# Kernel optimization log

Hardware: AMD Instinct MI355X
Metric: run time of the kernel (lower is better)

Reference implementation:

```python
import jax, jax.numpy as jnp
import numpy as np

B, S, D, H = 2, 2048, 4096, 32
HD = D // H  # 128

def _rope(t, cos, sin):
    # t: [B,S,H,HD]; cos,sin: [S,HD//2]; interleaved complex pairs on last dim
    b, s, h, d = t.shape
    tr = t.reshape(b, s, h, d // 2, 2)
    x0, x1 = tr[..., 0], tr[..., 1]
    c = cos[None, :, None, :]
    sn = sin[None, :, None, :]
    o0 = x0 * c - x1 * sn
    o1 = x0 * sn + x1 * c
    return jnp.stack([o0, o1], axis=-1).reshape(b, s, h, d)

def setup_inputs() -> dict:
    key = jax.random.key(0)
    ks = jax.random.split(key, 6)
    x = jax.random.normal(ks[0], (B, S, D), dtype=jnp.float32)
    theta = 10000.0 ** (-jnp.arange(0, HD, 2, dtype=jnp.float32) / HD)  # [HD//2]
    ang = jnp.arange(S, dtype=jnp.float32)[:, None] * theta[None, :]    # [S, HD//2]
    freqs_cos, freqs_sin = jnp.cos(ang), jnp.sin(ang)
    # additive causal mask [S,S]
    mask = jnp.where(jnp.triu(jnp.ones((S, S), dtype=bool), k=1), -1e9, 0.0).astype(jnp.float32)
    std = 1.0 / np.sqrt(D)
    wq = jax.random.normal(ks[1], (D, D), dtype=jnp.float32) * std
    wk = jax.random.normal(ks[2], (D, D), dtype=jnp.float32) * std
    wv = jax.random.normal(ks[3], (D, D), dtype=jnp.float32) * std
    wo = jax.random.normal(ks[4], (D, D), dtype=jnp.float32) * std
    return {"x": x, "freqs_cos": freqs_cos, "freqs_sin": freqs_sin, "mask": mask,
            "wq": wq, "wk": wk, "wv": wv, "wo": wo, "start_pos": 0}

def reference(x, freqs_cos, freqs_sin, mask, wq, wk, wv, wo, start_pos):
    b, s, d = x.shape
    # Linear layers: torch nn.Linear stores weight [out,in] -> x @ W.T
    xq = (x @ wq.T).reshape(b, s, H, HD)
    xk = (x @ wk.T).reshape(b, s, H, HD)
    xv = (x @ wv.T).reshape(b, s, H, HD)
    xq = _rope(xq, freqs_cos, freqs_sin)
    xk = _rope(xk, freqs_cos, freqs_sin)
    # prefill (start_pos=0): cache slice [:, :s] == xk, xv
    scale = 1.0 / jnp.sqrt(jnp.float32(HD))
    scores = jnp.einsum("bqhd,bkhd->bhqk", xq, xk) * scale + mask[None, None, :, :]
    probs = jax.nn.softmax(scores, axis=-1)
    out = jnp.einsum("bhqk,bkhd->bqhd", probs, xv).reshape(b, s, d)
    return out @ wo.T
```

## Files before the change

### kernel.cpp

```cpp
#include <hip/hip_runtime.h>
#include <hip/hip_bf16.h>
#include <math.h>

typedef unsigned short u16;
typedef __bf16 bf16x8 __attribute__((ext_vector_type(8)));
typedef float f32x4 __attribute__((ext_vector_type(4)));

#define B_  2
#define S_  2048
#define D_  4096
#define H_  32
#define HD_ 128

__device__ __forceinline__ unsigned rne_bf16(float x) {
  unsigned u = __float_as_uint(x);
  return (u + 0x7fffu + ((u >> 16) & 1u)) >> 16;
}

__device__ __forceinline__ void async16(void* lds_p, const void* g) {
  __builtin_amdgcn_global_load_lds(
      (__attribute__((address_space(1))) void*)(g),
      (__attribute__((address_space(3))) void*)(lds_p), 16, 0, 0);
}

__global__ __launch_bounds__(256) void convert_bf16(
    const float* __restrict__ src, u16* __restrict__ dst, int n8) {
  int i = blockIdx.x * 256 + threadIdx.x;
  if (i >= n8) return;
  const float4* s = (const float4*)src + (size_t)i * 2;
  float4 a = s[0], b = s[1];
  uint4 o;
  o.x = rne_bf16(a.x) | (rne_bf16(a.y) << 16);
  o.y = rne_bf16(a.z) | (rne_bf16(a.w) << 16);
  o.z = rne_bf16(b.x) | (rne_bf16(b.y) << 16);
  o.w = rne_bf16(b.z) | (rne_bf16(b.w) << 16);
  ((uint4*)dst)[i] = o;
}

__global__ __launch_bounds__(256) void convert_bf16_x4(
    const float* __restrict__ s0, const float* __restrict__ s1,
    const float* __restrict__ s2, const float* __restrict__ s3,
    u16* __restrict__ d0, u16* __restrict__ d1,
    u16* __restrict__ d2, u16* __restrict__ d3) {
  const int per = (B_ * S_ * D_) / 8 / 256;
  const int which = blockIdx.x / per;
  const int i = (blockIdx.x % per) * 256 + threadIdx.x;
  const float* src = which == 0 ? s0 : which == 1 ? s1 : which == 2 ? s2 : s3;
  u16* dst = which == 0 ? d0 : which == 1 ? d1 : which == 2 ? d2 : d3;
  const float4* s = (const float4*)src + (size_t)i * 2;
  float4 a = s[0], b = s[1];
  uint4 o;
  o.x = rne_bf16(a.x) | (rne_bf16(a.y) << 16);
  o.y = rne_bf16(a.z) | (rne_bf16(a.w) << 16);
  o.z = rne_bf16(b.x) | (rne_bf16(b.y) << 16);
  o.w = rne_bf16(b.z) | (rne_bf16(b.w) << 16);
  ((uint4*)dst)[i] = o;
}

template <int MODE>
__global__ __launch_bounds__(256, 3) void gemm_bt(
    const u16* __restrict__ A, const u16* __restrict__ Bw,
    u16* __restrict__ outB, float* __restrict__ outF,
    const float* __restrict__ fc, const float* __restrict__ fs) {
  __shared__ __align__(16) u16 lds[24576];
  const int tid  = threadIdx.x;
  const int lane = tid & 63;
  const int wave = tid >> 6;
  const int lm   = lane & 15, quad = lane >> 4;
  const int mr = (wave >> 1) * 64, nc = (wave & 1) * 64;
  const int K = 4096;
  const int NT = K / 32;

  const int bid = blockIdx.y * 32 + blockIdx.x;
  const int xg = bid & 7, l = bid >> 3;
  const int m0 = (((xg & 3) * 8) + (l & 7)) * 128;
  const int n0 = (((xg >> 2) * 16) + (l >> 3)) * 128;

  const int ca = tid, cb = tid + 256;
  const int ra = ca >> 2, ga = ((ca & 3) ^ ((ca >> 3) & 3)) * 8;
  const int rb = cb >> 2, gb = ((cb & 3) ^ ((cb >> 3) & 3)) * 8;
  const u16* Ag0 = A + (size_t)(m0 + ra) * K + ga;
  const u16* Ag1 = A + (size_t)(m0 + rb) * K + gb;
  const u16* Bg0 = Bw + (size_t)(n0 + ra) * K + ga;
  const u16* Bg1 = Bw + (size_t)(n0 + rb) * K + gb;

  const int koff = (quad ^ ((lm >> 1) & 3)) * 8;

  f32x4 acc[4][4] = {};

#define GSTAGE(BUF, T) do {                                   \
    u16* Ld_ = lds + (BUF) * 8192;                            \
    const size_t ko_ = (size_t)(T) * 32;                      \
    async16(&Ld_[ca * 8], Ag0 + ko_);                         \
    async16(&Ld_[cb * 8], Ag1 + ko_);                         \
    async16(&Ld_[4096 + ca * 8], Bg0 + ko_);                  \
    async16(&Ld_[4096 + cb * 8], Bg1 + ko_);                  \
  } while (0)

  GSTAGE(0, 0);
  GSTAGE(1, 1);
  asm volatile("s_waitcnt vmcnt(4)" ::: "memory");
  asm volatile("s_barrier" ::: "memory");

  int rbuf = 0, sbuf = 2;
  for (int t = 0; t < NT; ++t) {
    const u16* As = lds + rbuf * 8192;
    const u16* Bs = As + 4096;
    if (t + 2 < NT) GSTAGE(sbuf, t + 2);
    bf16x8 af[4], bfr[4];
#pragma unroll
    for (int i = 0; i < 4; ++i) af[i] = *(const bf16x8*)&As[(mr + i * 16 + lm) * 32 + koff];
#pragma unroll
    for (int j = 0; j < 4; ++j) bfr[j] = *(const bf16x8*)&Bs[(nc + j * 16 + lm) * 32 + koff];
#pragma unroll
    for (int i = 0; i < 4; ++i)
#pragma unroll
      for (int j = 0; j < 4; ++j)
        acc[i][j] = __builtin_amdgcn_mfma_f32_16x16x32_bf16(af[i], bfr[j], acc[i][j], 0, 0, 0);
    if (t < NT - 1) {
      if (t + 2 < NT) {
        asm volatile("s_waitcnt vmcnt(4)" ::: "memory");
      } else {
        asm volatile("s_waitcnt vmcnt(0)" ::: "memory");
      }
      asm volatile("s_barrier" ::: "memory");
    }
    rbuf = rbuf == 2 ? 0 : rbuf + 1;
    sbuf = sbuf == 2 ? 0 : sbuf + 1;
  }
#undef GSTAGE

  if (MODE == 1) {
#pragma unroll
    for (int i = 0; i < 4; ++i) {
      const int mbase = m0 + mr + i * 16 + quad * 4;
#pragma unroll
      for (int j = 0; j < 4; ++j) {
        const int n = n0 + nc + j * 16 + lm;
        const int h = n >> 7, d = n & 127, ir = d >> 1;
#pragma unroll
        for (int r = 0; r < 4; ++r) {
          const int m = mbase + r;
          const int s = m & (S_ - 1);
          const int bb = m >> 11;
          float v = acc[i][j][r];
          float p = __shfl_xor(v, 1);
          float cv = fc[s * (HD_ / 2) + ir];
          float sv = fs[s * (HD_ / 2) + ir];
          float o = ((lane & 1) == 0) ? (v * cv - p * sv) : (p * sv + v * cv);
          float po = __shfl_xor(o, 1);
          if ((lane & 1) == 0) {
            unsigned pkt = rne_bf16(o) | (rne_bf16(po) << 16);
            size_t idx = (((size_t)(bb * H_ + h) * S_ + s) * HD_ + d) >> 1;
            ((unsigned*)outB)[idx] = pkt;
          }
        }
      }
    }
  } else if (MODE == 3) {
#pragma unroll
    for (int i = 0; i < 4; ++i) {
      const int mbase = m0 + mr + i * 16 + quad * 4;
      const int s0 = mbase & (S_ - 1);
      const int bb = mbase >> 11;
#pragma unroll
      for (int j = 0; j < 4; ++j) {
        const int n = n0 + nc + j * 16 + lm;
        const int h = n >> 7, d = n & 127;
        uint2 pkt;
        pkt.x = rne_bf16(acc[i][j][0]) | (rne_bf16(acc[i][j][1]) << 16);
        pkt.y = rne_bf16(acc[i][j][2]) | (rne_bf16(acc[i][j][3]) << 16);
        size_t idx = ((size_t)(bb * H_ + h) * HD_ + d) * S_ + s0;
        *(uint2*)&outB[idx] = pkt;
      }
    }
  } else {
#pragma unroll
    for (int i = 0; i < 4; ++i) {
      const int mbase = m0 + mr + i * 16 + quad * 4;
#pragma unroll
      for (int j = 0; j < 4; ++j) {
        const int n = n0 + nc + j * 16 + lm;
#pragma unroll
        for (int r = 0; r < 4; ++r) outF[(size_t)(mbase + r) * D_ + n] = acc[i][j][r];
      }
    }
  }
}

__global__ __launch_bounds__(256, 2) void flash_attn(
    const u16* __restrict__ Qb, const u16* __restrict__ Kb,
    const u16* __restrict__ Vtb, u16* __restrict__ attn) {
  __shared__ __align__(16) u16 lds[32768];

  const int tid = threadIdx.x;
  const int lane = tid & 63, w = tid >> 6;
  const int lm = lane & 15, quad = lane >> 4;
  const int qb = 15 - blockIdx.x;
  const int bh = blockIdx.y;
  const int bb = bh >> 5, h = bh & 31;

  const u16* Qg = Qb + ((size_t)bh * S_ + qb * 128 + w * 32) * HD_;
  const u16* Kg = Kb + (size_t)bh * S_ * HD_;
  const u16* Vg = Vtb + (size_t)bh * HD_ * S_;

  const u16* kp[4];
  const u16* vp[4];
#pragma unroll
  for (int it = 0; it < 4; ++it) {
    int c = tid + 256 * it;
    int kr = c >> 4, kc = (c & 15) ^ (kr & 15);
    kp[it] = Kg + (size_t)kr * HD_ + kc * 8;
    int vr = c >> 3, vc = (c & 7) ^ (vr & 7);
    vp[it] = Vg + (size_t)vr * S_ + vc * 8;
  }

  bf16x8 qf[2][4];
#pragma unroll
  for (int qt = 0; qt < 2; ++qt)
#pragma unroll
    for (int dk = 0; dk < 4; ++dk)
      qf[qt][dk] = *(const bf16x8*)(Qg + (size_t)(qt * 16 + lm) * HD_ + dk * 32 + quad * 8);

  f32x4 accO[8][2] = {};
  float m_run[2] = {-1e30f, -1e30f}, l_run[2] = {0.f, 0.f};
  const float scale = 0.08838834764831845f;
  const float THR = 90.50966799187809f;
  const int nkt = 2 * qb + 2;
  const int qg0 = qb * 128 + w * 32;
  const int wq_max = qg0 + 31;

#pragma unroll
  for (int it = 0; it < 4; ++it) {
    async16(&lds[(tid + 256 * it) * 8], kp[it]);
    async16(&lds[8192 + (tid + 256 * it) * 8], vp[it]);
  }

  for (int kt = 0; kt < nkt; ++kt) {
    const int k0 = kt * 64;
    const int cur = (kt & 1) * 16384;
    __syncthreads();
    if (kt + 1 < nkt) {
      const int nxt = cur ^ 16384;
      const size_t koK = (size_t)(kt + 1) * 64 * HD_;
      const size_t koV = (size_t)(kt + 1) * 64;
#pragma unroll
      for (int it = 0; it < 4; ++it) {
        async16(&lds[nxt + (tid + 256 * it) * 8], kp[it] + koK);
        async16(&lds[nxt + 8192 + (tid + 256 * it) * 8], vp[it] + koV);
      }
    }
    if (k0 <= wq_max) {
      const u16* Ks = lds + cur;
      const u16* Vts = lds + cur + 8192;
      f32x4 sacc[2][4] = {};
#pragma unroll
      for (int dk = 0; dk < 4; ++dk) {
        bf16x8 kf[4];
#pragma unroll
        for (int t = 0; t < 4; ++t) {
          int row = (t >> 1) * 32 + ((lm >> 2) * 8) + ((t & 1) * 4) + (lm & 3);
          int ch = (dk * 4 + quad) ^ (row & 15);
          kf[t] = *(const bf16x8*)&Ks[(row * 16 + ch) * 8];
        }
        __builtin_amdgcn_s_setprio(1);
#pragma unroll
        for (int t = 0; t < 4; ++t)
#pragma unroll
          for (int qt = 0; qt < 2; ++qt)
            sacc[qt][t] = __builtin_amdgcn_mfma_f32_16x16x32_bf16(kf[t], qf[qt][dk], sacc[qt][t], 0, 0, 0);
        __builtin_amdgcn_s_setprio(0);
      }
      if (k0 + 63 > qg0) {
#pragma unroll
        for (int qt = 0; qt < 2; ++qt) {
          int q = qg0 + qt * 16 + lm;
#pragma unroll
          for (int t = 0; t < 4; ++t) {
            int kb = k0 + (t >> 1) * 32 + quad * 8 + (t & 1) * 4;
#pragma unroll
            for (int r = 0; r < 4; ++r)
              if (kb + r > q) sacc[qt][t][r] = -1e30f;
          }
        }
      }
      float tmaxv[2];
#pragma unroll
      for (int qt = 0; qt < 2; ++qt) {
        float tmax = sacc[qt][0][0];
#pragma unroll
        for (int t = 0; t < 4; ++t)
#pragma unroll
          for (int r = 0; r < 4; ++r) tmax = fmaxf(tmax, sacc[qt][t][r]);
        tmax = fmaxf(tmax, __shfl_xor(tmax, 16));
        tmax = fmaxf(tmax, __shfl_xor(tmax, 32));
        tmaxv[qt] = tmax;
      }
      bool needl = (tmaxv[0] - m_run[0] > THR) || (tmaxv[1] - m_run[1] > THR);
      if (__any(needl)) {
#pragma unroll
        for (int qt = 0; qt < 2; ++qt) {
          float mnew = fmaxf(m_run[qt], tmaxv[qt]);
          float alpha = __expf((m_run[qt] - mnew) * scale);
          m_run[qt] = mnew;
          l_run[qt] *= alpha;
#pragma unroll
          for (int dt = 0; dt < 8; ++dt)
#pragma unroll
            for (int r = 0; r < 4; ++r) accO[dt][qt][r] *= alpha;
        }
      }
      bf16x8 pf[2][2];
#pragma unroll
      for (int qt = 0; qt < 2; ++qt) {
        float ms = m_run[qt] * scale;
        float rs = 0.f;
#pragma unroll
        for (int t = 0; t < 4; ++t)
#pragma unroll
          for (int r = 0; r < 4; ++r) {
            float p = __expf(fmaf(sacc[qt][t][r], scale, -ms));
            sacc[qt][t][r] = p;
            rs += p;
          }
        rs += __shfl_xor(rs, 16);
        rs += __shfl_xor(rs, 32);
        l_run[qt] += rs;
#pragma unroll
        for (int kc = 0; kc < 2; ++kc)
#pragma unroll
          for (int j = 0; j < 4; ++j) {
            pf[kc][qt][j]     = (__bf16)sacc[qt][2 * kc][j];
            pf[kc][qt][j + 4] = (__bf16)sacc[qt][2 * kc + 1][j];
          }
      }
      __builtin_amdgcn_s_setprio(1);
#pragma unroll
      for (int kc = 0; kc < 2; ++kc)
#pragma unroll
        for (int dt = 0; dt < 8; ++dt) {
          int row = dt * 16 + lm;
          int ch = (kc * 4 + quad) ^ (row & 7);
          bf16x8 vf = *(const bf16x8*)&Vts[(row * 8 + ch) * 8];
#pragma unroll
          for (int qt = 0; qt < 2; ++qt)
            accO[dt][qt] = __builtin_amdgcn_mfma_f32_16x16x32_bf16(vf, pf[kc][qt], accO[dt][qt], 0, 0, 0);
        }
      __builtin_amdgcn_s_setprio(0);
    }
  }

  __syncthreads();
  u16* Et = lds;
  float inv[2] = {1.f / l_run[0], 1.f / l_run[1]};
#pragma unroll
  for (int dt = 0; dt < 8; ++dt)
#pragma unroll
    for (int qt = 0; qt < 2; ++qt) {
      const int rowq = w * 32 + qt * 16 + lm;
#pragma unroll
      for (int rp = 0; rp < 2; ++rp) {
        float a0 = accO[dt][qt][rp * 2] * inv[qt];
        float a1 = accO[dt][qt][rp * 2 + 1] * inv[qt];
        unsigned pkt = rne_bf16(a0) | (rne_bf16(a1) << 16);
        *(unsigned*)&Et[rowq * 136 + dt * 16 + quad * 4 + rp * 2] = pkt;
      }
    }
  const int rloc = w * 32 + (lane >> 1);
  const int half = lane & 1;
  const size_t gbase = (size_t)(bb * S_ + qb * 128 + rloc) * D_ + h * 128 + half * 64;
#pragma unroll
  for (int k = 0; k < 8; ++k) {
    uint4 vv = *(const uint4*)&Et[rloc * 136 + half * 64 + k * 8];
    *(uint4*)&attn[gbase + k * 8] = vv;
  }
}

extern "C" void kernel_launch(void* const* d_in, const int* in_sizes, int n_in,
                              void* d_out, int out_size, void* d_ws, size_t ws_size,
                              hipStream_t stream) {
  const float* x  = (const float*)d_in[0];
  const float* fc = (const float*)d_in[1];
  const float* fs = (const float*)d_in[2];
  const float* wq = (const float*)d_in[4];
  const float* wk = (const float*)d_in[5];
  const float* wv = (const float*)d_in[6];
  const float* wo = (const float*)d_in[7];
  float* out = (float*)d_out;

  char* ws = (char*)d_ws;
  const size_t SZ = (size_t)B_ * S_ * D_ * 2;
  u16* xb  = (u16*)(ws);
  u16* wqb = (u16*)(ws + SZ);
  u16* wkb = (u16*)(ws + 2 * SZ);
  u16* wvb = (u16*)(ws + 3 * SZ);
  u16* Qb  = (u16*)(ws + 4 * SZ);
  u16* Kb  = (u16*)(ws + 5 * SZ);
  u16* Vtb = (u16*)(ws + 6 * SZ);
  u16* attn = xb;
  u16* wob  = wqb;

  dim3 blk(256);
  const int n8 = (B_ * S_ * D_) / 8;
  convert_bf16_x4<<<4 * (n8 / 256), blk, 0, stream>>>(x, wq, wk, wv, xb, wqb, wkb, wvb);

  dim3 g1(32, 32);
  gemm_bt<1><<<g1, blk, 0, stream>>>(xb, wqb, Qb, nullptr, fc, fs);
  gemm_bt<1><<<g1, blk, 0, stream>>>(xb, wkb, Kb, nullptr, fc, fs);
  gemm_bt<3><<<g1, blk, 0, stream>>>(xb, wvb, Vtb, nullptr, nullptr, nullptr);

  dim3 g2(16, 64);
  flash_attn<<<g2, blk, 0, stream>>>(Qb, Kb, Vtb, attn);

  convert_bf16<<<n8 / 256, blk, 0, stream>>>(wo, wob, n8);
  gemm_bt<4><<<g1, blk, 0, stream>>>(attn, wob, nullptr, out, nullptr, nullptr);
}
```

Baseline: 1.135 ms.

## Shrink LDS in GEMM and attention to raise occupancy

The GEMM drops from a three-stage to a two-stage LDS pipeline with a full barrier each k-step, cutting shared memory from 48KB to 32KB. The attention kernel double-buffers only K and single-buffers V, loading V for the current tile during QK^T and softmax, with an extra wait and barrier before PV. LDS drops to 48KB and launch bounds go to 3 blocks per CU. This trades prefetch depth and extra synchronisation for higher occupancy, and risks exposing load latency.

```diff
diff --git a/kernel.cpp b/kernel.cpp
--- a/kernel.cpp
+++ b/kernel.cpp
@@ -62,7 +62,7 @@
     const u16* __restrict__ A, const u16* __restrict__ Bw,
     u16* __restrict__ outB, float* __restrict__ outF,
     const float* __restrict__ fc, const float* __restrict__ fs) {
-  __shared__ __align__(16) u16 lds[24576];
+  __shared__ __align__(16) u16 lds[16384];
   const int tid  = threadIdx.x;
   const int lane = tid & 63;
   const int wave = tid >> 6;
@@ -88,25 +88,23 @@
 
   f32x4 acc[4][4] = {};
 
-#define GSTAGE(BUF, T) do {                                   \
-    u16* Ld_ = lds + (BUF) * 8192;                            \
-    const size_t ko_ = (size_t)(T) * 32;                      \
-    async16(&Ld_[ca * 8], Ag0 + ko_);                         \
-    async16(&Ld_[cb * 8], Ag1 + ko_);                         \
-    async16(&Ld_[4096 + ca * 8], Bg0 + ko_);                  \
-    async16(&Ld_[4096 + cb * 8], Bg1 + ko_);                  \
-  } while (0)
-
-  GSTAGE(0, 0);
-  GSTAGE(1, 1);
-  asm volatile("s_waitcnt vmcnt(4)" ::: "memory");
-  asm volatile("s_barrier" ::: "memory");
-
-  int rbuf = 0, sbuf = 2;
+  async16(&lds[ca * 8], Ag0);
+  async16(&lds[cb * 8], Ag1);
+  async16(&lds[4096 + ca * 8], Bg0);
+  async16(&lds[4096 + cb * 8], Bg1);
+  __syncthreads();
+
   for (int t = 0; t < NT; ++t) {
-    const u16* As = lds + rbuf * 8192;
+    const u16* As = lds + (t & 1) * 8192;
     const u16* Bs = As + 4096;
-    if (t + 2 < NT) GSTAGE(sbuf, t + 2);
+    if (t < NT - 1) {
+      u16* Ld = lds + ((t + 1) & 1) * 8192;
+      const size_t ko = (size_t)(t + 1) * 32;
+      async16(&Ld[ca * 8], Ag0 + ko);
+      async16(&Ld[cb * 8], Ag1 + ko);
+      async16(&Ld[4096 + ca * 8], Bg0 + ko);
+      async16(&Ld[4096 + cb * 8], Bg1 + ko);
+    }
     bf16x8 af[4], bfr[4];
 #pragma unroll
     for (int i = 0; i < 4; ++i) af[i] = *(const bf16x8*)&As[(mr + i * 16 + lm) * 32 + koff];
@@ -117,18 +115,8 @@
 #pragma unroll
       for (int j = 0; j < 4; ++j)
         acc[i][j] = __builtin_amdgcn_mfma_f32_16x16x32_bf16(af[i], bfr[j], acc[i][j], 0, 0, 0);
-    if (t < NT - 1) {
-      if (t + 2 < NT) {
-        asm volatile("s_waitcnt vmcnt(4)" ::: "memory");
-      } else {
-        asm volatile("s_waitcnt vmcnt(0)" ::: "memory");
-      }
-      asm volatile("s_barrier" ::: "memory");
-    }
-    rbuf = rbuf == 2 ? 0 : rbuf + 1;
-    sbuf = sbuf == 2 ? 0 : sbuf + 1;
+    __syncthreads();
   }
-#undef GSTAGE
 
   if (MODE == 1) {
 #pragma unroll
@@ -188,10 +176,10 @@
   }
 }
 
-__global__ __launch_bounds__(256, 2) void flash_attn(
+__global__ __launch_bounds__(256, 3) void flash_attn(
     const u16* __restrict__ Qb, const u16* __restrict__ Kb,
     const u16* __restrict__ Vtb, u16* __restrict__ attn) {
-  __shared__ __align__(16) u16 lds[32768];
+  __shared__ __align__(16) u16 lds[24576];
 
   const int tid = threadIdx.x;
   const int lane = tid & 63, w = tid >> 6;
@@ -231,29 +219,30 @@
   const int wq_max = qg0 + 31;
 
 #pragma unroll
-  for (int it = 0; it < 4; ++it) {
+  for (int it = 0; it < 4; ++it)
     async16(&lds[(tid + 256 * it) * 8], kp[it]);
-    async16(&lds[8192 + (tid + 256 * it) * 8], vp[it]);
-  }
 
   for (int kt = 0; kt < nkt; ++kt) {
     const int k0 = kt * 64;
-    const int cur = (kt & 1) * 16384;
+    const int curK = (kt & 1) * 8192;
     __syncthreads();
-    if (kt + 1 < nkt) {
-      const int nxt = cur ^ 16384;
-      const size_t koK = (size_t)(kt + 1) * 64 * HD_;
-      const size_t koV = (size_t)(kt + 1) * 64;
-#pragma unroll
-      for (int it = 0; it < 4; ++it) {
-        async16(&lds[nxt + (tid + 256 * it) * 8], kp[it] + koK);
-        async16(&lds[nxt + 8192 + (tid + 256 * it) * 8], vp[it] + koV);
-      }
-    }
-    if (k0 <= wq_max) {
-      const u16* Ks = lds + cur;
-      const u16* Vts = lds + cur + 8192;
-      f32x4 sacc[2][4] = {};
+    {
+      const size_t koV = (size_t)kt * 64;
+#pragma unroll
+      for (int it = 0; it < 4; ++it)
+        async16(&lds[16384 + (tid + 256 * it) * 8], vp[it] + koV);
+      if (kt + 1 < nkt) {
+        const size_t koK = (size_t)(kt + 1) * 64 * HD_;
+#pragma unroll
+        for (int it = 0; it < 4; ++it)
+          async16(&lds[(curK ^ 8192) + (tid + 256 * it) * 8], kp[it] + koK);
+      }
+    }
+    const bool live = (k0 <= wq_max);
+    f32x4 sacc[2][4] = {};
+    bf16x8 pf[2][2];
+    if (live) {
+      const u16* Ks = lds + curK;
 #pragma unroll
       for (int dk = 0; dk < 4; ++dk) {
         bf16x8 kf[4];
@@ -310,7 +299,6 @@
             for (int r = 0; r < 4; ++r) accO[dt][qt][r] *= alpha;
         }
       }
-      bf16x8 pf[2][2];
 #pragma unroll
       for (int qt = 0; qt < 2; ++qt) {
         float ms = m_run[qt] * scale;
@@ -334,6 +322,15 @@
             pf[kc][qt][j + 4] = (__bf16)sacc[qt][2 * kc + 1][j];
           }
       }
+    }
+    if (kt + 1 < nkt) {
+      asm volatile("s_waitcnt vmcnt(4)" ::: "memory");
+    } else {
+      asm volatile("s_waitcnt vmcnt(0)" ::: "memory");
+    }
+    __builtin_amdgcn_s_barrier();
+    if (live) {
+      const u16* Vts = lds + 16384;
       __builtin_amdgcn_s_setprio(1);
 #pragma unroll
       for (int kc = 0; kc < 2; ++kc)
```

New measurement: 1.305 ms. 1.15x slower.
